# Optimization experiments

Hardware: AMD Instinct MI355X
Metric: run time of the kernel (lower is better)

The kernel has to match this reference:

```python
import jax, jax.numpy as jnp
import numpy as np

LN_EPS = 1e-5

def _layernorm(x):
    # LayerNorm over last dim, no affine params (elementwise_affine=False)
    mu = jnp.mean(x, axis=-1, keepdims=True)
    var = jnp.var(x, axis=-1, keepdims=True)
    return (x - mu) / jnp.sqrt(var + LN_EPS)

def setup_inputs() -> dict:
    key = jax.random.key(0)
    k1, k2 = jax.random.split(key)
    B, S, D_IN, D_OUT = 4, 2048, 4096, 4096
    x = jax.random.normal(k1, (B, S, D_IN), dtype=jnp.float32)
    # kaiming-uniform-ish init scale (exact distribution irrelevant for correctness baseline)
    bound = 1.0 / np.sqrt(D_IN)
    weight = jax.random.uniform(k2, (D_OUT, D_IN), dtype=jnp.float32, minval=-bound, maxval=bound)
    return {"x": x, "weight": weight}

def reference(x, weight):
    # weight mean-centering and scalar scale beta
    w_centered = weight - jnp.mean(weight)
    beta = jnp.mean(jnp.abs(w_centered))
    x_norm = _layernorm(x)
    w_bin = jnp.sign(w_centered)                       # [D_out, D_in] in {-1,0,+1}
    out = jnp.einsum('bsi,oi->bso', x_norm, w_bin)     # dense GEMM on binarized weights
    return out * beta
```

## Files before the change

kernel.cpp:

```cpp
#include <hip/hip_runtime.h>
#include <hip/hip_bf16.h>
#include <stdint.h>


typedef __bf16 bf16x8 __attribute__((ext_vector_type(8)));
typedef float f32x4 __attribute__((ext_vector_type(4)));

#define LDS_BUF 65536


__device__ __forceinline__ void gl_lds16(const void* g, void* l) {
  __builtin_amdgcn_global_load_lds(
      (const __attribute__((address_space(1))) void*)g,
      (__attribute__((address_space(3))) void*)l,
      16, 0, 0);
}

__device__ __forceinline__ unsigned short f2bf_rne(float f) {
  unsigned int u = __float_as_uint(f);
  unsigned int r = (u + 0x7FFFu + ((u >> 16) & 1u)) >> 16;
  return (unsigned short)r;
}

__device__ __forceinline__ float wave_red(float v) {
#pragma unroll
  for (int o = 32; o > 0; o >>= 1) v += __shfl_down(v, o, 64);
  return v;
}

__device__ __forceinline__ float block_red(float v) {
  __shared__ float tmp[4];
  const int wave = threadIdx.x >> 6, lane = threadIdx.x & 63;
  v = wave_red(v);
  if (lane == 0) tmp[wave] = v;
  __syncthreads();
  float r = 0.f;
  if (threadIdx.x == 0) r = tmp[0] + tmp[1] + tmp[2] + tmp[3];
  return r;
}


__global__ void zero_kernel(float* p) {
  if (threadIdx.x < 8) p[threadIdx.x] = 0.f;
}

__global__ __launch_bounds__(256) void wsum_kernel(const float* __restrict__ w,
                                                   float* __restrict__ scal, int n4) {
  int idx = blockIdx.x * 256 + threadIdx.x;
  int stride = gridDim.x * 256;
  const float4* w4 = (const float4*)w;
  float s = 0.f;
  for (int i = idx; i < n4; i += stride) {
    float4 a = w4[i];
    s += a.x + a.y + a.z + a.w;
  }
  float tot = block_red(s);
  if (threadIdx.x == 0) atomicAdd(&scal[0], tot);
}

__global__ __launch_bounds__(256) void wbin_kernel(const float* __restrict__ w,
                                                   float* __restrict__ scal,
                                                   unsigned short* __restrict__ wb,
                                                   int n4, float inv_n) {
  const float mean = scal[0] * inv_n;
  int idx = blockIdx.x * 256 + threadIdx.x;
  int stride = gridDim.x * 256;
  const float4* w4 = (const float4*)w;
  ushort4* wb4 = (ushort4*)wb;
  float sa = 0.f;
  for (int i = idx; i < n4; i += stride) {
    float4 a = w4[i];
    float dx = a.x - mean, dy = a.y - mean, dz = a.z - mean, dw = a.w - mean;
    sa += fabsf(dx) + fabsf(dy) + fabsf(dz) + fabsf(dw);
    ushort4 o;
    o.x = dx > 0.f ? 0x3F80u : (dx < 0.f ? 0xBF80u : 0u);
    o.y = dy > 0.f ? 0x3F80u : (dy < 0.f ? 0xBF80u : 0u);
    o.z = dz > 0.f ? 0x3F80u : (dz < 0.f ? 0xBF80u : 0u);
    o.w = dw > 0.f ? 0x3F80u : (dw < 0.f ? 0xBF80u : 0u);
    wb4[i] = o;
  }
  float tot = block_red(sa);
  if (threadIdx.x == 0) atomicAdd(&scal[1], tot);
}

__global__ __launch_bounds__(256) void ln_kernel(const float* __restrict__ x,
                                                 __bf16* __restrict__ xn) {
  const int row = blockIdx.x;
  const float4* xr = (const float4*)(x + (size_t)row * 4096);
  const int tid = threadIdx.x;
  float4 v[4];
  float s = 0.f, ss = 0.f;
#pragma unroll
  for (int t = 0; t < 4; t++) {
    float4 a = xr[t * 256 + tid];
    v[t] = a;
    s += a.x + a.y + a.z + a.w;
    ss += a.x * a.x + a.y * a.y + a.z * a.z + a.w * a.w;
  }
#pragma unroll
  for (int o = 32; o > 0; o >>= 1) {
    s += __shfl_down(s, o, 64);
    ss += __shfl_down(ss, o, 64);
  }
  __shared__ float rs[8];
  const int wave = tid >> 6, lane = tid & 63;
  if (lane == 0) { rs[wave] = s; rs[4 + wave] = ss; }
  __syncthreads();
  s = rs[0] + rs[1] + rs[2] + rs[3];
  ss = rs[4] + rs[5] + rs[6] + rs[7];
  const float mu = s * (1.0f / 4096.0f);
  const float var = ss * (1.0f / 4096.0f) - mu * mu;
  const float rstd = rsqrtf(var + 1e-5f);
  ushort4* xw = (ushort4*)((unsigned short*)xn + (size_t)row * 4096);
#pragma unroll
  for (int t = 0; t < 4; t++) {
    float4 a = v[t];
    ushort4 o;
    o.x = f2bf_rne((a.x - mu) * rstd);
    o.y = f2bf_rne((a.y - mu) * rstd);
    o.z = f2bf_rne((a.z - mu) * rstd);
    o.w = f2bf_rne((a.w - mu) * rstd);
    xw[t * 256 + tid] = o;
  }
}


__global__ __launch_bounds__(512, 2) void gemm_kernel(
    const __bf16* __restrict__ A, const __bf16* __restrict__ Bm,
    float* __restrict__ C, const float* __restrict__ scal,
    float beta_scale, int M, int N, int K) {
  extern __shared__ __align__(16) char sm[];

  const int tid = threadIdx.x;
  const int wave = tid >> 6, lane = tid & 63;
  const int wm = wave >> 2, wn = wave & 3;
  const int fr = lane & 15, hi4 = lane >> 4;

  const int nwg = gridDim.x;
  const int swz = (blockIdx.x & 7) * (nwg >> 3) + (blockIdx.x >> 3);
  const int TM = M >> 8;
  const int tm = swz % TM, tn = swz / TM;
  const int rowBase = tm << 8, colBase = tn << 8;

  const int s = (tid & 7) ^ ((tid >> 3) & 7);
  const int rb = ((tid >> 2) & ~1) | (s >> 2);
  const int colOff = (s & 3) << 3;
  const __bf16* srcA0 = A + (size_t)(rowBase + (rb & 63) + ((rb >> 6) << 7)) * K + colOff;
  const __bf16* srcB0 = Bm + (size_t)(colBase + rb) * K + colOff;
  const int waveOff = wave << 10;

  int abase = (wm << 12) + (fr << 6) + (hi4 << 4);
  abase ^= ((abase >> 7) & 7) << 4;
  int bbase = ((wn >> 1) << 13) + ((wn & 1) << 12) + (fr << 6) + (hi4 << 4);
  bbase ^= ((bbase >> 7) & 7) << 4;

  char* const buf0 = sm;
  char* const buf1 = sm + LDS_BUF;

  auto stA = [&](char* buf, int k, int qm, int kt) {
    gl_lds16(srcA0 + (size_t)(qm << 6) * K + (kt + (k << 5)),
             buf + (k << 14) + (qm << 13) + waveOff);
  };
  auto stB = [&](char* buf, int k, int half, int kt) {
    gl_lds16(srcB0 + (size_t)(half << 7) * K + (kt + (k << 5)),
             buf + 32768 + (k << 14) + (half << 13) + waveOff);
  };

  f32x4 acc[8][4];
#pragma unroll
  for (int i = 0; i < 8; i++)
#pragma unroll
    for (int j = 0; j < 4; j++) acc[i][j] = (f32x4){0.f, 0.f, 0.f, 0.f};

  const int NT = K >> 6;

  stA(buf0, 0, 0, 0); stA(buf0, 0, 1, 0); stB(buf0, 0, 0, 0); stB(buf0, 0, 1, 0);
  stA(buf0, 1, 0, 0); stA(buf0, 1, 1, 0); stB(buf0, 1, 0, 0); stB(buf0, 1, 1, 0);
  stA(buf1, 0, 0, 64); stA(buf1, 0, 1, 64); stB(buf1, 0, 0, 64);
  stA(buf1, 1, 0, 64); stB(buf1, 0, 1, 64);
  asm volatile("s_waitcnt vmcnt(5)" ::: "memory");
  asm volatile("s_barrier" ::: "memory");

  for (int T = 0; T < NT; ++T) {
    char* const bc = (T & 1) ? buf1 : buf0;
    char* const bo = (T & 1) ? buf0 : buf1;
    const int kt1 = ((T + 1 < NT) ? T + 1 : NT - 1) << 6;
    const int kt2 = ((T + 2 < NT) ? T + 2 : NT - 1) << 6;

    bf16x8 a[4], b[4];

#pragma unroll
    for (int i = 0; i < 4; i++) a[i] = *(const bf16x8*)(bc + abase + (i << 10));
#pragma unroll
    for (int j = 0; j < 4; j++) b[j] = *(const bf16x8*)(bc + 32768 + bbase + (j << 10));
    stA(bo, 1, 1, kt1); stB(bo, 1, 0, kt1); stB(bo, 1, 1, kt1);
    asm volatile("s_barrier" ::: "memory");
    asm volatile("s_waitcnt lgkmcnt(0)" ::: "memory");
    __builtin_amdgcn_s_setprio(1);
#pragma unroll
    for (int i = 0; i < 4; i++)
#pragma unroll
      for (int j = 0; j < 4; j++)
        acc[i][j] = __builtin_amdgcn_mfma_f32_16x16x32_bf16(a[i], b[j], acc[i][j], 0, 0, 0);
    __builtin_amdgcn_s_setprio(0);
    asm volatile("s_barrier" ::: "memory");

#pragma unroll
    for (int i = 0; i < 4; i++) a[i] = *(const bf16x8*)(bc + (1 << 13) + abase + (i << 10));
    stA(bc, 0, 0, kt2);
    asm volatile("s_barrier" ::: "memory");
    asm volatile("s_waitcnt lgkmcnt(0)" ::: "memory");
    __builtin_amdgcn_s_setprio(1);
#pragma unroll
    for (int i = 0; i < 4; i++)
#pragma unroll
      for (int j = 0; j < 4; j++)
        acc[4 + i][j] = __builtin_amdgcn_mfma_f32_16x16x32_bf16(a[i], b[j], acc[4 + i][j], 0, 0, 0);
    __builtin_amdgcn_s_setprio(0);
    asm volatile("s_barrier" ::: "memory");

#pragma unroll
    for (int i = 0; i < 4; i++) a[i] = *(const bf16x8*)(bc + (1 << 14) + abase + (i << 10));
#pragma unroll
    for (int j = 0; j < 4; j++) b[j] = *(const bf16x8*)(bc + 32768 + (1 << 14) + bbase + (j << 10));
    stA(bc, 0, 1, kt2); stB(bc, 0, 0, kt2);
    asm volatile("s_barrier" ::: "memory");
    asm volatile("s_waitcnt lgkmcnt(0)" ::: "memory");
    __builtin_amdgcn_s_setprio(1);
#pragma unroll
    for (int i = 0; i < 4; i++)
#pragma unroll
      for (int j = 0; j < 4; j++)
        acc[i][j] = __builtin_amdgcn_mfma_f32_16x16x32_bf16(a[i], b[j], acc[i][j], 0, 0, 0);
    __builtin_amdgcn_s_setprio(0);
    asm volatile("s_barrier" ::: "memory");

#pragma unroll
    for (int i = 0; i < 4; i++) a[i] = *(const bf16x8*)(bc + (1 << 14) + (1 << 13) + abase + (i << 10));
    stA(bc, 1, 0, kt2); stB(bc, 0, 1, kt2);
    asm volatile("s_barrier" ::: "memory");
    asm volatile("s_waitcnt lgkmcnt(0)" ::: "memory");
    __builtin_amdgcn_s_setprio(1);
#pragma unroll
    for (int i = 0; i < 4; i++)
#pragma unroll
      for (int j = 0; j < 4; j++)
        acc[4 + i][j] = __builtin_amdgcn_mfma_f32_16x16x32_bf16(a[i], b[j], acc[4 + i][j], 0, 0, 0);
    __builtin_amdgcn_s_setprio(0);
    asm volatile("s_waitcnt vmcnt(5)" ::: "memory");
    asm volatile("s_barrier" ::: "memory");
  }

  asm volatile("s_waitcnt vmcnt(0)" ::: "memory");

  const float beta = scal[1] * beta_scale;
  const int orow0 = rowBase + (wm << 7) + (hi4 << 2);
  const int ocol = colBase + (wn << 6) + fr;
#pragma unroll
  for (int mf = 0; mf < 8; mf++)
#pragma unroll
    for (int j = 0; j < 4; j++)
#pragma unroll
      for (int r = 0; r < 4; r++)
        C[(size_t)(orow0 + mf * 16 + r) * N + (ocol + j * 16)] = acc[mf][j][r] * beta;
}


extern "C" void kernel_launch(void* const* d_in, const int* in_sizes, int n_in,
                              void* d_out, int out_size, void* d_ws, size_t ws_size,
                              hipStream_t stream) {
  const float* x = (const float*)d_in[0];
  const float* w = (const float*)d_in[1];
  float* out = (float*)d_out;

  const int K = 4096;
  const int M = in_sizes[0] / K;
  const int N = in_sizes[1] / K;
  const int nw = N * K;
  const float inv_nw = 1.0f / (float)nw;

  char* ws = (char*)d_ws;
  float* scal = (float*)ws;
  __bf16* wbin = (__bf16*)(ws + 256);
  __bf16* xn = (__bf16*)(ws + 256 + (size_t)nw * 2);

  static int attr_done = 0;
  if (!attr_done) {
    hipFuncSetAttribute((const void*)gemm_kernel,
                        hipFuncAttributeMaxDynamicSharedMemorySize, 2 * LDS_BUF);
    attr_done = 1;
  }

  zero_kernel<<<1, 64, 0, stream>>>(scal);
  wsum_kernel<<<1024, 256, 0, stream>>>(w, scal, nw / 4);
  wbin_kernel<<<1024, 256, 0, stream>>>(w, scal, (unsigned short*)wbin, nw / 4, inv_nw);
  ln_kernel<<<M, 256, 0, stream>>>(x, xn);
  const int nwg = (M >> 8) * (N >> 8);
  gemm_kernel<<<dim3(nwg), 512, 2 * LDS_BUF, stream>>>(xn, wbin, out, scal, inv_nw, M, N, K);
}
```

Baseline: 572.7 us.

## Double-buffer LDS fragment reads in registers to overlap with MFMA phases

Restructures the GEMM main loop so each phase loads the next phase's A/B fragments from LDS into a second register set before running the current MFMA block. Explicit lgkmcnt waits go away, with sched_barrier fences added around the MFMA groups. The loop is unrolled by two with constant buffer pointers to drop the per-iteration buffer selects. This is meant to hide LDS read latency behind matrix math, at the cost of more registers and reliance on compiler-inserted waits, plus an assumption that NT is even.

New measurement: 588.3 us. +2.7%, slower.

```diff
diff --git a/kernel.cpp b/kernel.cpp
--- a/kernel.cpp
+++ b/kernel.cpp
@@ -181,74 +181,76 @@
   asm volatile("s_waitcnt vmcnt(5)" ::: "memory");
   asm volatile("s_barrier" ::: "memory");
 
-  for (int T = 0; T < NT; ++T) {
-    char* const bc = (T & 1) ? buf1 : buf0;
-    char* const bo = (T & 1) ? buf0 : buf1;
+  auto tile = [&](char* bc, char* bo, int T) {
     const int kt1 = ((T + 1 < NT) ? T + 1 : NT - 1) << 6;
     const int kt2 = ((T + 2 < NT) ? T + 2 : NT - 1) << 6;
-
-    bf16x8 a[4], b[4];
-
-#pragma unroll
-    for (int i = 0; i < 4; i++) a[i] = *(const bf16x8*)(bc + abase + (i << 10));
-#pragma unroll
-    for (int j = 0; j < 4; j++) b[j] = *(const bf16x8*)(bc + 32768 + bbase + (j << 10));
+    bf16x8 aA[4], aB[4], bA[4], bB[4];
+
+#pragma unroll
+    for (int i = 0; i < 4; i++) aA[i] = *(const bf16x8*)(bc + abase + (i << 10));
+#pragma unroll
+    for (int j = 0; j < 4; j++) bA[j] = *(const bf16x8*)(bc + 32768 + bbase + (j << 10));
     stA(bo, 1, 1, kt1); stB(bo, 1, 0, kt1); stB(bo, 1, 1, kt1);
+#pragma unroll
+    for (int i = 0; i < 4; i++) aB[i] = *(const bf16x8*)(bc + (1 << 13) + abase + (i << 10));
+    __builtin_amdgcn_sched_barrier(0);
+    __builtin_amdgcn_s_setprio(1);
+#pragma unroll
+    for (int i = 0; i < 4; i++)
+#pragma unroll
+      for (int j = 0; j < 4; j++)
+        acc[i][j] = __builtin_amdgcn_mfma_f32_16x16x32_bf16(aA[i], bA[j], acc[i][j], 0, 0, 0);
+    __builtin_amdgcn_s_setprio(0);
+    __builtin_amdgcn_sched_barrier(0);
     asm volatile("s_barrier" ::: "memory");
-    asm volatile("s_waitcnt lgkmcnt(0)" ::: "memory");
+
+    stA(bc, 0, 0, kt2);
+#pragma unroll
+    for (int i = 0; i < 4; i++) aA[i] = *(const bf16x8*)(bc + (1 << 14) + abase + (i << 10));
+#pragma unroll
+    for (int j = 0; j < 4; j++) bB[j] = *(const bf16x8*)(bc + 32768 + (1 << 14) + bbase + (j << 10));
+    __builtin_amdgcn_sched_barrier(0);
     __builtin_amdgcn_s_setprio(1);
 #pragma unroll
     for (int i = 0; i < 4; i++)
 #pragma unroll
       for (int j = 0; j < 4; j++)
-        acc[i][j] = __builtin_amdgcn_mfma_f32_16x16x32_bf16(a[i], b[j], acc[i][j], 0, 0, 0);
+        acc[4 + i][j] = __builtin_amdgcn_mfma_f32_16x16x32_bf16(aB[i], bA[j], acc[4 + i][j], 0, 0, 0);
     __builtin_amdgcn_s_setprio(0);
+    __builtin_amdgcn_sched_barrier(0);
     asm volatile("s_barrier" ::: "memory");
 
-#pragma unroll
-    for (int i = 0; i < 4; i++) a[i] = *(const bf16x8*)(bc + (1 << 13) + abase + (i << 10));
-    stA(bc, 0, 0, kt2);
+    stA(bc, 0, 1, kt2); stB(bc, 0, 0, kt2);
+#pragma unroll
+    for (int i = 0; i < 4; i++) aB[i] = *(const bf16x8*)(bc + (1 << 14) + (1 << 13) + abase + (i << 10));
+    __builtin_amdgcn_sched_barrier(0);
+    __builtin_amdgcn_s_setprio(1);
+#pragma unroll
+    for (int i = 0; i < 4; i++)
+#pragma unroll
+      for (int j = 0; j < 4; j++)
+        acc[i][j] = __builtin_amdgcn_mfma_f32_16x16x32_bf16(aA[i], bB[j], acc[i][j], 0, 0, 0);
+    __builtin_amdgcn_s_setprio(0);
+    __builtin_amdgcn_sched_barrier(0);
     asm volatile("s_barrier" ::: "memory");
-    asm volatile("s_waitcnt lgkmcnt(0)" ::: "memory");
+
+    stA(bc, 1, 0, kt2); stB(bc, 0, 1, kt2);
+    asm volatile("s_waitcnt vmcnt(5)" ::: "memory");
+    __builtin_amdgcn_sched_barrier(0);
     __builtin_amdgcn_s_setprio(1);
 #pragma unroll
     for (int i = 0; i < 4; i++)
 #pragma unroll
       for (int j = 0; j < 4; j++)
-        acc[4 + i][j] = __builtin_amdgcn_mfma_f32_16x16x32_bf16(a[i], b[j], acc[4 + i][j], 0, 0, 0);
+        acc[4 + i][j] = __builtin_amdgcn_mfma_f32_16x16x32_bf16(aB[i], bB[j], acc[4 + i][j], 0, 0, 0);
     __builtin_amdgcn_s_setprio(0);
+    __builtin_amdgcn_sched_barrier(0);
     asm volatile("s_barrier" ::: "memory");
-
-#pragma unroll
-    for (int i = 0; i < 4; i++) a[i] = *(const bf16x8*)(bc + (1 << 14) + abase + (i << 10));
-#pragma unroll
-    for (int j = 0; j < 4; j++) b[j] = *(const bf16x8*)(bc + 32768 + (1 << 14) + bbase + (j << 10));
-    stA(bc, 0, 1, kt2); stB(bc, 0, 0, kt2);
-    asm volatile("s_barrier" ::: "memory");
-    asm volatile("s_waitcnt lgkmcnt(0)" ::: "memory");
-    __builtin_amdgcn_s_setprio(1);
-#pragma unroll
-    for (int i = 0; i < 4; i++)
-#pragma unroll
-      for (int j = 0; j < 4; j++)
-        acc[i][j] = __builtin_amdgcn_mfma_f32_16x16x32_bf16(a[i], b[j], acc[i][j], 0, 0, 0);
-    __builtin_amdgcn_s_setprio(0);
-    asm volatile("s_barrier" ::: "memory");
-
-#pragma unroll
-    for (int i = 0; i < 4; i++) a[i] = *(const bf16x8*)(bc + (1 << 14) + (1 << 13) + abase + (i << 10));
-    stA(bc, 1, 0, kt2); stB(bc, 0, 1, kt2);
-    asm volatile("s_barrier" ::: "memory");
-    asm volatile("s_waitcnt lgkmcnt(0)" ::: "memory");
-    __builtin_amdgcn_s_setprio(1);
-#pragma unroll
-    for (int i = 0; i < 4; i++)
-#pragma unroll
-      for (int j = 0; j < 4; j++)
-        acc[4 + i][j] = __builtin_amdgcn_mfma_f32_16x16x32_bf16(a[i], b[j], acc[4 + i][j], 0, 0, 0);
-    __builtin_amdgcn_s_setprio(0);
-    asm volatile("s_waitcnt vmcnt(5)" ::: "memory");
-    asm volatile("s_barrier" ::: "memory");
+  };
+
+  for (int T = 0; T < NT; T += 2) {
+    tile(buf0, buf1, T);
+    tile(buf1, buf0, T + 1);
   }
 
   asm volatile("s_waitcnt vmcnt(0)" ::: "memory");
```
